# Kernel optimization log

Measured on AMD Instinct MI355X. Metric: run time of the kernel, lower is better.

## Reference

```python
import jax, jax.numpy as jnp
import numpy as np

B, T, C, H, N = 4, 4096, 1024, 16, 64
D_DECAY, D_AAA, D_MV, D_GATE = 64, 64, 32, 160
EPS_GN = 1e-5 * 8 ** 2  # GroupNorm eps = 1e-5 * head_size_divisor**2


def _k(i):
    return jax.random.fold_in(jax.random.key(0), i)


def setup_inputs():
    p = {}
    p["x"] = jax.random.normal(_k(1), (B, T, C), jnp.float32)
    p["v_first"] = jax.random.normal(_k(2), (B, T, C), jnp.float32)
    for i, name in enumerate(["x_r", "x_w", "x_k", "x_v", "x_a", "x_g"]):
        p[name] = jax.random.uniform(_k(10 + i), (1, 1, C), jnp.float32)
    p["w0"] = jnp.linspace(-7.0, -2.0, C, dtype=jnp.float32).reshape(1, 1, C) + 0.5
    p["w1"] = jax.random.normal(_k(20), (C, D_DECAY), jnp.float32) * 0.02
    p["w2"] = jax.random.normal(_k(21), (D_DECAY, C), jnp.float32) * 0.02
    p["a0"] = jax.random.normal(_k(22), (1, 1, C), jnp.float32) * 0.02
    p["a1"] = jax.random.normal(_k(23), (C, D_AAA), jnp.float32) * 0.02
    p["a2"] = jax.random.normal(_k(24), (D_AAA, C), jnp.float32) * 0.02
    p["v0"] = jnp.ones((1, 1, C), jnp.float32)
    p["v1"] = jax.random.normal(_k(25), (C, D_MV), jnp.float32) * 0.02
    p["v2"] = jax.random.normal(_k(26), (D_MV, C), jnp.float32) * 0.02
    p["g1"] = jax.random.normal(_k(27), (C, D_GATE), jnp.float32) * 0.02
    p["g2"] = jax.random.normal(_k(28), (D_GATE, C), jnp.float32) * 0.02
    p["k_k"] = jnp.full((1, 1, C), 0.85, jnp.float32)
    p["k_a"] = jnp.ones((1, 1, C), jnp.float32)
    p["r_k"] = jax.random.normal(_k(29), (H, N), jnp.float32) * 0.02
    s = 0.5 / C ** 0.5
    p["Wr"] = jax.random.uniform(_k(30), (C, C), jnp.float32, -s, s)
    p["Wk"] = jax.random.uniform(_k(31), (C, C), jnp.float32, -0.1 * s, 0.1 * s)
    p["Wv"] = jax.random.uniform(_k(32), (C, C), jnp.float32, -s, s)
    p["Wo"] = jax.random.uniform(_k(33), (C, C), jnp.float32, -s, s)
    p["ln_w"] = jnp.ones((C,), jnp.float32)
    p["ln_b"] = jnp.zeros((C,), jnp.float32)
    p["alpha"] = jnp.array(0.5, jnp.float32)
    return p


def _wkv_scan(ins, reverse):
    # ins: tuple of time-major (T,B,H,N) arrays: r, decay, k, v, a, b
    def step(S, inp):
        r_t, d_t, k_t, v_t, a_t, b_t = inp
        sa = jnp.einsum('bhij,bhj->bhi', S, a_t)  # in-context removal term
        S = (S * d_t[:, :, None, :]
             + sa[..., None] * b_t[:, :, None, :]
             + v_t[..., None] * k_t[:, :, None, :])
        return S, jnp.einsum('bhij,bhj->bhi', S, r_t)
    S0 = jnp.zeros((B, H, N, N), jnp.float32)
    return jax.lax.scan(step, S0, ins, reverse=reverse)[1]


def reference(x, v_first, x_r, x_w, x_k, x_v, x_a, x_g, w0, w1, w2, a0, a1, a2,
              v0, v1, v2, g1, g2, k_k, k_a, r_k, Wr, Wk, Wv, Wo, ln_w, ln_b, alpha):
    xx = jnp.pad(x, ((0, 0), (1, 0), (0, 0)))[:, :T, :] - x  # token shift
    xr = x + xx * x_r
    xw = x + xx * x_w
    xk = x + xx * x_k
    xv = x + xx * x_v
    xa = x + xx * x_a
    xg = x + xx * x_g
    r = xr @ Wr.T
    w = -jax.nn.softplus(-(w0 + jnp.tanh(xw @ w1) @ w2)) - 0.5
    k = xk @ Wk.T
    v = xv @ Wv.T
    v = v + (v_first - v) * jax.nn.sigmoid(v0 + (xv @ v1) @ v2)  # layer_id != 0
    a = jax.nn.sigmoid(a0 + (xa @ a1) @ a2)
    g = jax.nn.sigmoid(xg @ g1) @ g2
    kk = (k * k_k).reshape(B, T, H, N)
    kk = kk / jnp.maximum(jnp.linalg.norm(kk, axis=-1, keepdims=True), 1e-12)
    k = k * (1.0 + (a - 1.0) * k_a)
    rh = r.reshape(B, T, H, N)
    kh = k.reshape(B, T, H, N)
    vh = v.reshape(B, T, H, N)
    dec = jnp.exp(-jnp.exp(w.reshape(B, T, H, N)))  # per-channel decay
    ah = -kk
    bh = kk * a.reshape(B, T, H, N)
    tm = lambda z: jnp.transpose(z, (1, 0, 2, 3))  # -> (T,B,H,N)
    ins = (tm(rh), tm(dec), tm(kh), tm(vh), tm(ah), tm(bh))
    y_f = _wkv_scan(ins, reverse=False)
    y_b = _wkv_scan(ins, reverse=True)
    y = alpha * y_f + (1.0 - alpha) * y_b  # bidirectional blend (alpha)
    y = jnp.transpose(y, (1, 0, 2, 3))  # (B,T,H,N)
    mu = y.mean(-1, keepdims=True)
    var = y.var(-1, keepdims=True)
    y = (y - mu) / jnp.sqrt(var + EPS_GN)  # GroupNorm(H groups)
    y = y * ln_w.reshape(1, 1, H, N) + ln_b.reshape(1, 1, H, N)
    y = y + (rh * kh * r_k).sum(-1, keepdims=True) * vh
    out = (y.reshape(B, T, C) * g) @ Wo.T
    return (out, v_first)
```

## Files before the change

kernel.cpp:

```cpp
#include <hip/hip_runtime.h>
#include <hip/hip_bf16.h>
#include <math.h>

#define BB 4
#define TT 4096
#define CC 1024
#define HH 16
#define NN 64
#define BT (BB*TT)
#define EPS_GN 6.4e-4f
#define TMAX (TT-1)
#define LCH 64
#define STR 68
#define STR2 36

typedef __attribute__((ext_vector_type(8))) short bf16x8;
typedef __attribute__((ext_vector_type(4))) float f32x4;

__device__ __forceinline__ float sigmoidf_(float x) {
    return 1.0f / (1.0f + expf(-x));
}

__device__ __forceinline__ float waveReduceSum(float v) {
    #pragma unroll
    for (int off = 32; off > 0; off >>= 1)
        v += __shfl_xor(v, off, 64);
    return v;
}

__device__ __forceinline__ unsigned short f2bf(float f) {
    unsigned u = __float_as_uint(f);
    u += 0x7FFFu + ((u >> 16) & 1u);
    return (unsigned short)(u >> 16);
}
__device__ __forceinline__ float bf2f(unsigned short h) {
    return __uint_as_float(((unsigned)h) << 16);
}

__device__ __forceinline__ void gll16(const unsigned short* g, unsigned short* l) {
    __builtin_amdgcn_global_load_lds(
        (__attribute__((address_space(1))) void*)(g),
        (__attribute__((address_space(3))) void*)(l), 16, 0, 0);
}

template<int SA0,int SA1,int SB0,int SB1>
__device__ __forceinline__ void gemm64(const float* __restrict__ A,
                                       const float* __restrict__ B,
                                       float acc[4][4], int tr, int tc) {
    #pragma unroll 2
    for (int kx = 0; kx < 64; kx += 4) {
        float a_[4][4];
        if (SA0 == 1) {
            #pragma unroll
            for (int kk = 0; kk < 4; kk++) {
                float4 t = *(const float4*)&A[tr + (kx + kk) * SA1];
                a_[0][kk] = t.x; a_[1][kk] = t.y; a_[2][kk] = t.z; a_[3][kk] = t.w;
            }
        } else {
            #pragma unroll
            for (int r = 0; r < 4; r++) {
                float4 t = *(const float4*)&A[(tr + r) * SA0 + kx];
                a_[r][0] = t.x; a_[r][1] = t.y; a_[r][2] = t.z; a_[r][3] = t.w;
            }
        }
        float b_[4][4];
        if (SB0 == 1) {
            #pragma unroll
            for (int kk = 0; kk < 4; kk++) {
                float4 t = *(const float4*)&B[tc + (kx + kk) * SB1];
                b_[0][kk] = t.x; b_[1][kk] = t.y; b_[2][kk] = t.z; b_[3][kk] = t.w;
            }
        } else {
            #pragma unroll
            for (int cq = 0; cq < 4; cq++) {
                float4 t = *(const float4*)&B[(tc + cq) * SB0 + kx];
                b_[cq][0] = t.x; b_[cq][1] = t.y; b_[cq][2] = t.z; b_[cq][3] = t.w;
            }
        }
        #pragma unroll
        for (int r = 0; r < 4; r++)
            #pragma unroll
            for (int cq = 0; cq < 4; cq++)
                #pragma unroll
                for (int kk = 0; kk < 4; kk++)
                    acc[r][cq] = fmaf(a_[r][kk], b_[cq][kk], acc[r][cq]);
    }
}

__global__ __launch_bounds__(256) void conv_split_x6(
    const float* __restrict__ X,
    const float* __restrict__ mr, const float* __restrict__ mk,
    const float* __restrict__ mv, const float* __restrict__ mw,
    const float* __restrict__ ma, const float* __restrict__ mg,
    unsigned short* __restrict__ rH, unsigned short* __restrict__ rL,
    unsigned short* __restrict__ kH, unsigned short* __restrict__ kL,
    unsigned short* __restrict__ vH, unsigned short* __restrict__ vL,
    unsigned short* __restrict__ wH, unsigned short* __restrict__ wL,
    unsigned short* __restrict__ aH, unsigned short* __restrict__ aL,
    unsigned short* __restrict__ gH, unsigned short* __restrict__ gL)
{
    int g = blockIdx.x * 256 + threadIdx.x;
    int m = g >> 7;
    int k = (g & 127) * 8;
    const float* px = X + (size_t)m * CC + k;
    float xv8[8], pv[8];
    {
        float4 x0 = *(const float4*)px;
        float4 x1 = *(const float4*)(px + 4);
        xv8[0]=x0.x; xv8[1]=x0.y; xv8[2]=x0.z; xv8[3]=x0.w;
        xv8[4]=x1.x; xv8[5]=x1.y; xv8[6]=x1.z; xv8[7]=x1.w;
    }
    if ((m & (TT - 1)) == 0) {
        #pragma unroll
        for (int j = 0; j < 8; j++) pv[j] = 0.f;
    } else {
        float4 p0 = *(const float4*)(px - CC);
        float4 p1 = *(const float4*)(px - CC + 4);
        pv[0]=p0.x; pv[1]=p0.y; pv[2]=p0.z; pv[3]=p0.w;
        pv[4]=p1.x; pv[5]=p1.y; pv[6]=p1.z; pv[7]=p1.w;
    }
    const float* mixes[6] = {mr, mk, mv, mw, ma, mg};
    unsigned short* His[6] = {rH, kH, vH, wH, aH, gH};
    unsigned short* Los[6] = {rL, kL, vL, wL, aL, gL};
    for (int s = 0; s < 6; s++) {
        float4 m0 = *(const float4*)(mixes[s] + k);
        float4 m1 = *(const float4*)(mixes[s] + k + 4);
        float mv8[8] = {m0.x,m0.y,m0.z,m0.w,m1.x,m1.y,m1.z,m1.w};
        unsigned short hi[8], lo[8];
        #pragma unroll
        for (int j = 0; j < 8; j++) {
            float a = xv8[j] + (pv[j] - xv8[j]) * mv8[j];
            hi[j] = f2bf(a);
            lo[j] = f2bf(a - bf2f(hi[j]));
        }
        uint4 H, L;
        H.x = (unsigned)hi[0] | ((unsigned)hi[1] << 16);
        H.y = (unsigned)hi[2] | ((unsigned)hi[3] << 16);
        H.z = (unsigned)hi[4] | ((unsigned)hi[5] << 16);
        H.w = (unsigned)hi[6] | ((unsigned)hi[7] << 16);
        L.x = (unsigned)lo[0] | ((unsigned)lo[1] << 16);
        L.y = (unsigned)lo[2] | ((unsigned)lo[3] << 16);
        L.z = (unsigned)lo[4] | ((unsigned)lo[5] << 16);
        L.w = (unsigned)lo[6] | ((unsigned)lo[7] << 16);
        *(uint4*)(His[s] + (size_t)g * 8) = H;
        *(uint4*)(Los[s] + (size_t)g * 8) = L;
    }
}

__global__ __launch_bounds__(256) void conv_w4(
    const float* __restrict__ Wr, const float* __restrict__ Wk,
    const float* __restrict__ Wv, const float* __restrict__ Wo,
    unsigned short* __restrict__ Hi, unsigned short* __restrict__ Lo)
{
    int g = blockIdx.x * 256 + threadIdx.x;
    int y = blockIdx.y;
    const float* W = (y == 0) ? Wr : (y == 1) ? Wk : (y == 2) ? Wv : Wo;
    size_t doff = (size_t)y * CC * CC;
    int m = g >> 7;
    int k = (g & 127) * 8;
    const float* px = W + (size_t)m * CC + k;
    float a[8];
    {
        float4 x0 = *(const float4*)px;
        float4 x1 = *(const float4*)(px + 4);
        a[0]=x0.x; a[1]=x0.y; a[2]=x0.z; a[3]=x0.w;
        a[4]=x1.x; a[5]=x1.y; a[6]=x1.z; a[7]=x1.w;
    }
    unsigned short hi[8], lo[8];
    #pragma unroll
    for (int j = 0; j < 8; j++) {
        hi[j] = f2bf(a[j]);
        lo[j] = f2bf(a[j] - bf2f(hi[j]));
    }
    uint4 H, L;
    H.x = (unsigned)hi[0] | ((unsigned)hi[1] << 16);
    H.y = (unsigned)hi[2] | ((unsigned)hi[3] << 16);
    H.z = (unsigned)hi[4] | ((unsigned)hi[5] << 16);
    H.w = (unsigned)hi[6] | ((unsigned)hi[7] << 16);
    L.x = (unsigned)lo[0] | ((unsigned)lo[1] << 16);
    L.y = (unsigned)lo[2] | ((unsigned)lo[3] << 16);
    L.z = (unsigned)lo[4] | ((unsigned)lo[5] << 16);
    L.w = (unsigned)lo[6] | ((unsigned)lo[7] << 16);
    *(uint4*)(Hi + doff + (size_t)g * 8) = H;
    *(uint4*)(Lo + doff + (size_t)g * 8) = L;
}

__global__ __launch_bounds__(256) void conv_w1y(
    const float* __restrict__ w1, const float* __restrict__ a1,
    const float* __restrict__ v1, const float* __restrict__ g1,
    unsigned short* __restrict__ w1th, unsigned short* __restrict__ w1tl,
    unsigned short* __restrict__ a1th, unsigned short* __restrict__ a1tl,
    unsigned short* __restrict__ v1th, unsigned short* __restrict__ v1tl,
    unsigned short* __restrict__ g1th, unsigned short* __restrict__ g1tl)
{
    const int y = blockIdx.y;
    const float* W = (y == 0) ? w1 : (y == 1) ? a1 : (y == 2) ? v1 : g1;
    unsigned short* Hi = (y == 0) ? w1th : (y == 1) ? a1th : (y == 2) ? v1th : g1th;
    unsigned short* Lo = (y == 0) ? w1tl : (y == 1) ? a1tl : (y == 2) ? v1tl : g1tl;
    const int N    = (y == 2) ? 32 : (y == 3) ? 160 : 64;
    const int Npad = (y == 3) ? 192 : 64;
    int idx = blockIdx.x * 256 + threadIdx.x;
    if (idx >= Npad * 128) return;
    int n = idx >> 7, k0 = (idx & 127) * 8;
    unsigned short h8[8], l8[8];
    #pragma unroll
    for (int j = 0; j < 8; j++) {
        int k = k0 + j;
        float v = (n < N) ? W[(size_t)k * N + n] : 0.f;
        h8[j] = f2bf(v);
        l8[j] = f2bf(v - bf2f(h8[j]));
    }
    uint4 H, L;
    H.x = (unsigned)h8[0] | ((unsigned)h8[1] << 16);
    H.y = (unsigned)h8[2] | ((unsigned)h8[3] << 16);
    H.z = (unsigned)h8[4] | ((unsigned)h8[5] << 16);
    H.w = (unsigned)h8[6] | ((unsigned)h8[7] << 16);
    L.x = (unsigned)l8[0] | ((unsigned)l8[1] << 16);
    L.y = (unsigned)l8[2] | ((unsigned)l8[3] << 16);
    L.z = (unsigned)l8[4] | ((unsigned)l8[5] << 16);
    L.w = (unsigned)l8[6] | ((unsigned)l8[7] << 16);
    *(uint4*)(Hi + (size_t)n * CC + k0) = H;
    *(uint4*)(Lo + (size_t)n * CC + k0) = L;
}

__global__ __launch_bounds__(256) void conv_w2y(
    const float* __restrict__ w2, const float* __restrict__ a2,
    const float* __restrict__ v2, const float* __restrict__ g2,
    unsigned short* __restrict__ w2th, unsigned short* __restrict__ w2tl,
    unsigned short* __restrict__ a2th, unsigned short* __restrict__ a2tl,
    unsigned short* __restrict__ v2th, unsigned short* __restrict__ v2tl,
    unsigned short* __restrict__ g2th, unsigned short* __restrict__ g2tl)
{
    const int y = blockIdx.y;
    const float* W = (y == 0) ? w2 : (y == 1) ? a2 : (y == 2) ? v2 : g2;
    unsigned short* Hi = (y == 0) ? w2th : (y == 1) ? a2th : (y == 2) ? v2th : g2th;
    unsigned short* Lo = (y == 0) ? w2tl : (y == 1) ? a2tl : (y == 2) ? v2tl : g2tl;
    const int K  = (y == 2) ? 32 : (y == 3) ? 160 : 64;
    const int Kp = (y == 3) ? 192 : 64;
    int idx = blockIdx.x * 256 + threadIdx.x;
    int nk8 = Kp >> 3;
    if (idx >= CC * nk8) return;
    int n = idx / nk8, k0 = (idx - n * nk8) * 8;
    unsigned short h8[8], l8[8];
    #pragma unroll
    for (int j = 0; j < 8; j++) {
        int k = k0 + j;
        float v = (k < K) ? W[(size_t)k * CC + n] : 0.f;
        h8[j] = f2bf(v);
        l8[j] = f2bf(v - bf2f(h8[j]));
    }
    uint4 H, L;
    H.x = (unsigned)h8[0] | ((unsigned)h8[1] << 16);
    H.y = (unsigned)h8[2] | ((unsigned)h8[3] << 16);
    H.z = (unsigned)h8[4] | ((unsigned)h8[5] << 16);
    H.w = (unsigned)h8[6] | ((unsigned)h8[7] << 16);
    L.x = (unsigned)l8[0] | ((unsigned)l8[1] << 16);
    L.y = (unsigned)l8[2] | ((unsigned)l8[3] << 16);
    L.z = (unsigned)l8[4] | ((unsigned)l8[5] << 16);
    L.w = (unsigned)l8[6] | ((unsigned)l8[7] << 16);
    *(uint4*)(Hi + (size_t)n * Kp + k0) = H;
    *(uint4*)(Lo + (size_t)n * Kp + k0) = L;
}

__global__ __launch_bounds__(256, 3) void gemm_split_bf16(
    const unsigned short* __restrict__ A0h, const unsigned short* __restrict__ A0l,
    const unsigned short* __restrict__ A1h, const unsigned short* __restrict__ A1l,
    const unsigned short* __restrict__ A2h, const unsigned short* __restrict__ A2l,
    const unsigned short* __restrict__ W4h, const unsigned short* __restrict__ W4l,
    float* __restrict__ O0, float* __restrict__ O1, float* __restrict__ O2,
    int wbase)
{
    __shared__ __align__(16) unsigned short lds[4][128 * 32];
    const int sel = blockIdx.y;
    const unsigned short* Ah = (sel == 0) ? A0h : (sel == 1) ? A1h : A2h;
    const unsigned short* Al = (sel == 0) ? A0l : (sel == 1) ? A1l : A2l;
    float* Out = (sel == 0) ? O0 : (sel == 1) ? O1 : O2;
    const unsigned short* Bh = W4h + (size_t)(wbase + sel) * CC * CC;
    const unsigned short* Bl = W4l + (size_t)(wbase + sel) * CC * CC;
    const int tid = threadIdx.x, lane = tid & 63, wave = tid >> 6;
    const int wm = (wave >> 1) * 64, wn = (wave & 1) * 64;
    const int wg = blockIdx.x;
    const int xcd = wg & 7;
    const int j = wg >> 3;
    const int m0 = ((j >> 3) * 8 + xcd) * 128;
    const int n0 = (j & 7) * 128;

    f32x4 acc[4][4];
    #pragma unroll
    for (int i = 0; i < 4; i++)
        #pragma unroll
        for (int jj = 0; jj < 4; jj++)
            acc[i][jj] = (f32x4){0.f, 0.f, 0.f, 0.f};

    for (int k0 = 0; k0 < CC; k0 += 32) {
        #pragma unroll
        for (int p = 0; p < 4; p++) {
            const unsigned short* sbase = (p == 0) ? Ah : (p == 1) ? Al
                                        : (p == 2) ? Bh : Bl;
            const int rbase = (p < 2) ? m0 : n0;
            #pragma unroll
            for (int i = 0; i < 2; i++) {
                int slot = i * 256 + wave * 64 + lane;
                int row = slot >> 2, gsl = slot & 3;
                const unsigned short* src = sbase
                    + (size_t)(rbase + row) * CC + k0 + ((gsl ^ (row & 3)) * 8);
                gll16(src, &lds[p][(size_t)(i * 256 + wave * 64) * 8]);
            }
        }
        __syncthreads();

        const int gk = lane >> 4;
        bf16x8 bhf[4], blf[4];
        #pragma unroll
        for (int nt = 0; nt < 4; nt++) {
            int col = wn + nt * 16 + (lane & 15);
            int el = col * 32 + ((gk ^ (col & 3)) * 8);
            bhf[nt] = *(const bf16x8*)&lds[2][el];
// ... 109 lines not shown
            #pragma unroll
            for (int nt = 0; nt < 2; nt++) {
                acc[mt][nt] = __builtin_amdgcn_mfma_f32_16x16x32_bf16(
                    ahf, bhf[nt], acc[mt][nt], 0, 0, 0);
                acc[mt][nt] = __builtin_amdgcn_mfma_f32_16x16x32_bf16(
                    alf, bhf[nt], acc[mt][nt], 0, 0, 0);
                acc[mt][nt] = __builtin_amdgcn_mfma_f32_16x16x32_bf16(
                    ahf, blf[nt], acc[mt][nt], 0, 0, 0);
            }
        }
        __syncthreads();
    }
    #pragma unroll
    for (int mt = 0; mt < 4; mt++)
        #pragma unroll
        for (int nt = 0; nt < 2; nt++) {
            int col = n0 + wn + nt * 16 + (lane & 15);
            #pragma unroll
            for (int r = 0; r < 4; r++) {
                int row = m0 + wm + mt * 16 + (lane >> 4) * 4 + r;
                float v = acc[mt][nt][r];
                if (epi == 1) v = tanhf(v);
                else if (epi == 2) v = sigmoidf_(v);
                unsigned short h = f2bf(v);
                size_t off = (size_t)row * Kp + col;
                Oh[off] = h;
                Ol[off] = f2bf(v - bf2f(h));
            }
        }
}

__global__ __launch_bounds__(256, 3) void lora2_mfma(
    const unsigned short* __restrict__ awh, const unsigned short* __restrict__ awl,
    const unsigned short* __restrict__ aah, const unsigned short* __restrict__ aal,
    const unsigned short* __restrict__ avh, const unsigned short* __restrict__ avl,
    const unsigned short* __restrict__ agh, const unsigned short* __restrict__ agl,
    const unsigned short* __restrict__ w2h, const unsigned short* __restrict__ w2l,
    const unsigned short* __restrict__ a2h, const unsigned short* __restrict__ a2l,
    const unsigned short* __restrict__ v2h, const unsigned short* __restrict__ v2l,
    const unsigned short* __restrict__ g2h, const unsigned short* __restrict__ g2l,
    const float* __restrict__ w0, const float* __restrict__ a0v,
    const float* __restrict__ v0v, const float* __restrict__ v_first,
    float* __restrict__ decb, float* __restrict__ ab,
    float* __restrict__ vbuf, float* __restrict__ gb)
{
    __shared__ __align__(16) unsigned short lds[24576];
    const int z = blockIdx.z;
    const unsigned short *Ah, *Al, *Bh, *Bl; int Kp;
    if (z == 0)      { Ah = awh; Al = awl; Bh = w2h; Bl = w2l; Kp = 64;  }
    else if (z == 1) { Ah = aah; Al = aal; Bh = a2h; Bl = a2l; Kp = 64;  }
    else if (z == 2) { Ah = avh; Al = avl; Bh = v2h; Bl = v2l; Kp = 64;  }
    else             { Ah = agh; Al = agl; Bh = g2h; Bl = g2l; Kp = 192; }

    const int tid = threadIdx.x, lane = tid & 63, wave = tid >> 6;
    const int wm = (wave >> 1) * 64, wn = (wave & 1) * 32;
    const int m0 = blockIdx.x * 128, n0 = blockIdx.y * 64;

    f32x4 acc[4][2];
    #pragma unroll
    for (int i = 0; i < 4; i++)
        #pragma unroll
        for (int jj = 0; jj < 2; jj++)
            acc[i][jj] = (f32x4){0.f, 0.f, 0.f, 0.f};

    for (int k0 = 0; k0 < Kp; k0 += 64) {
        #pragma unroll
        for (int p = 0; p < 2; p++) {
            const unsigned short* sbase = (p == 0) ? Ah : Al;
            #pragma unroll
            for (int i = 0; i < 4; i++) {
                int slot = i * 256 + wave * 64 + lane;
                int row = slot >> 3, gsl = slot & 7;
                const unsigned short* src = sbase
                    + (size_t)(m0 + row) * Kp + k0 + ((gsl ^ (row & 7)) * 8);
                gll16(src, &lds[(size_t)(p * 8192) + (size_t)(i * 256 + wave * 64) * 8]);
            }
        }
        #pragma unroll
        for (int p = 0; p < 2; p++) {
            const unsigned short* sbase = (p == 0) ? Bh : Bl;
            #pragma unroll
            for (int i = 0; i < 2; i++) {
                int slot = i * 256 + wave * 64 + lane;
                int row = slot >> 3, gsl = slot & 7;
                const unsigned short* src = sbase
                    + (size_t)(n0 + row) * Kp + k0 + ((gsl ^ (row & 7)) * 8);
                gll16(src, &lds[(size_t)(16384 + p * 4096) + (size_t)(i * 256 + wave * 64) * 8]);
            }
        }
        __syncthreads();

        #pragma unroll
        for (int ks = 0; ks < 2; ks++) {
            bf16x8 bhf[2], blf[2];
            #pragma unroll
            for (int nt = 0; nt < 2; nt++) {
                int col = wn + nt * 16 + (lane & 15);
                int gk = ks * 4 + (lane >> 4);
                int el = col * 64 + ((gk ^ (col & 7)) * 8);
                bhf[nt] = *(const bf16x8*)&lds[16384 + el];
                blf[nt] = *(const bf16x8*)&lds[20480 + el];
            }
            #pragma unroll
            for (int mt = 0; mt < 4; mt++) {
                int row = wm + mt * 16 + (lane & 15);
                int gk = ks * 4 + (lane >> 4);
                int el = row * 64 + ((gk ^ (row & 7)) * 8);
                bf16x8 ahf = *(const bf16x8*)&lds[el];
                bf16x8 alf = *(const bf16x8*)&lds[8192 + el];
                #pragma unroll
                for (int nt = 0; nt < 2; nt++) {
                    acc[mt][nt] = __builtin_amdgcn_mfma_f32_16x16x32_bf16(
                        ahf, bhf[nt], acc[mt][nt], 0, 0, 0);
                    acc[mt][nt] = __builtin_amdgcn_mfma_f32_16x16x32_bf16(
                        alf, bhf[nt], acc[mt][nt], 0, 0, 0);
                    acc[mt][nt] = __builtin_amdgcn_mfma_f32_16x16x32_bf16(
                        ahf, blf[nt], acc[mt][nt], 0, 0, 0);
                }
            }
        }
        __syncthreads();
    }
    float* cf = (float*)&lds[0];
    #pragma unroll
    for (int mt = 0; mt < 4; mt++)
        #pragma unroll
        for (int nt = 0; nt < 2; nt++)
            #pragma unroll
            for (int r = 0; r < 4; r++) {
                int row = wm + mt * 16 + (lane >> 4) * 4 + r;
                int col = wn + nt * 16 + (lane & 15);
                cf[row * 68 + col] = acc[mt][nt][r];
            }
    __syncthreads();
    #pragma unroll
    for (int i = 0; i < 8; i++) {
        int idx = tid + 256 * i;
        int row = idx >> 4, c4 = (idx & 15) * 4;
        float4 v = *(float4*)&cf[row * 68 + c4];
        int gm = m0 + row;
        int c = n0 + c4;
        size_t off = (size_t)gm * CC + c;
        if (z == 0) {
            float4 w0q = *(const float4*)(w0 + c);
            float4 o;
            o.x = expf(-expf(-log1pf(expf(-(w0q.x + v.x))) - 0.5f));
            o.y = expf(-expf(-log1pf(expf(-(w0q.y + v.y))) - 0.5f));
            o.z = expf(-expf(-log1pf(expf(-(w0q.z + v.z))) - 0.5f));
            o.w = expf(-expf(-log1pf(expf(-(w0q.w + v.w))) - 0.5f));
            *(float4*)&decb[off] = o;
        } else if (z == 1) {
            float4 a0q = *(const float4*)(a0v + c);
            float4 o;
            o.x = sigmoidf_(a0q.x + v.x);
            o.y = sigmoidf_(a0q.y + v.y);
            o.z = sigmoidf_(a0q.z + v.z);
            o.w = sigmoidf_(a0q.w + v.w);
            *(float4*)&ab[off] = o;
        } else if (z == 2) {
            float4 v0q = *(const float4*)(v0v + c);
            float4 vr = *(const float4*)&vbuf[off];
            float4 vf = *(const float4*)&v_first[off];
            float4 o;
            o.x = vr.x + (vf.x - vr.x) * sigmoidf_(v0q.x + v.x);
            o.y = vr.y + (vf.y - vr.y) * sigmoidf_(v0q.y + v.y);
            o.z = vr.z + (vf.z - vr.z) * sigmoidf_(v0q.z + v.z);
            o.w = vr.w + (vf.w - vr.w) * sigmoidf_(v0q.w + v.w);
            *(float4*)&vbuf[off] = o;
        } else {
            *(float4*)&gb[off] = v;
        }
    }
}

template<int CBT>
__global__ __launch_bounds__(256, 3) void wkvA(
    const float* __restrict__ kb, const float* __restrict__ ab,
    const float* __restrict__ vb, const float* __restrict__ decb,
    const float* __restrict__ k_k, const float* __restrict__ k_a,
    float* __restrict__ Gb, float* __restrict__ Ub,
    float* __restrict__ Bpb, float* __restrict__ Kpb,
    float* __restrict__ wcb, int cb)
{
    __shared__ __align__(16) float sA[64 * STR];
    __shared__ __align__(16) float sO[64 * STR];
    __shared__ __align__(16) float sT[64 * STR];
    __shared__ float sSeg[4][64];
    const int inst = blockIdx.x;
    const int bhd = inst / CBT, lc = inst % CBT;
    const int dir = bhd & 1, bh = bhd >> 1, b = bh >> 4, h = bh & 15;
    const int c64 = (cb * CBT + lc) * LCH;
    const int tid = threadIdx.x;
    const int lane = tid & 63, seg = tid >> 6;
    const int ch = h * 64 + lane;
    const size_t gbase = (size_t)inst * 4096;

    float loc[16];
    {
        float run = 1.f;
        #pragma unroll
        for (int i = 0; i < 16; i++) {
            int p = seg * 16 + i;
            int t = dir ? (TMAX - (c64 + p)) : (c64 + p);
            float d = decb[((size_t)(b * TT + t)) * CC + ch];
            run *= d; loc[i] = run;
        }
        sSeg[seg][lane] = run;
    }
    __syncthreads();
    float pre = 1.f;
    for (int s2 = 0; s2 < seg; ++s2) pre *= sSeg[s2][lane];
    float kreg[16];
    {
        const float kkl = k_k[ch], kal = k_a[ch];
        #pragma unroll
        for (int i = 0; i < 16; i++) {
            int p = seg * 16 + i;
            int t = dir ? (TMAX - (c64 + p)) : (c64 + p);
            size_t ra = ((size_t)(b * TT + t)) * CC + ch;
            float kraw = kb[ra], asig = ab[ra];
            float kkv = kraw * kkl;
            float s2 = waveReduceSum(kkv * kkv);
            float kkn = kkv / fmaxf(sqrtf(s2), 1e-12f);
            float wc = loc[i] * pre;
            float wx = (i == 0) ? pre : loc[i - 1] * pre;
            float apv = -kkn * wx;
            float bpv = kkn * asig / wc;
            float kpv = kraw * (1.f + (asig - 1.f) * kal) / wc;
            sA[lane * STR + p] = apv;
            sO[lane * STR + p] = bpv;
            kreg[i] = kpv;
            Gb[gbase + p * 64 + lane] = apv;
            Bpb[gbase + p * 64 + lane] = bpv;
            Kpb[gbase + p * 64 + lane] = kpv;
            wcb[gbase + p * 64 + lane] = wc;
        }
    }
    __syncthreads();

    const int tr = (tid >> 4) * 4, tc = (tid & 15) * 4;
    {
        float acc[4][4] = {};
        gemm64<1, STR, 1, STR>(sA, sO, acc, tr, tc);
        #pragma unroll
        for (int r = 0; r < 4; r++)
            #pragma unroll
            for (int cq = 0; cq < 4; cq++)
                sT[(tr + r) * STR + tc + cq] = (tc + cq < tr + r) ? acc[r][cq] : 0.f;
    }
    __syncthreads();
    #pragma unroll
    for (int i = 0; i < 16; i++)
        sO[lane * STR + seg * 16 + i] = kreg[i];
    __syncthreads();
    {
        float acc[4][4] = {};
        gemm64<1, STR, 1, STR>(sA, sO, acc, tr, tc);
        __syncthreads();
        #pragma unroll
        for (int r = 0; r < 4; r++)
            #pragma unroll
            for (int cq = 0; cq < 4; cq++)
                sA[(tr + r) * STR + tc + cq] = (tc + cq < tr + r) ? acc[r][cq] : 0.f;
    }
    __syncthreads();
    {
        float accY[4][4] = {};
        const float* vbase = vb + ((size_t)(b * TT + (dir ? (TMAX - c64) : c64))) * CC
                           + h * 64 + tc;
        const ptrdiff_t vstep = dir ? -(ptrdiff_t)CC : (ptrdiff_t)CC;
        #pragma unroll 2
        for (int j4 = 0; j4 < 64; j4 += 4) {
            float a_[4][4];
            #pragma unroll
            for (int r = 0; r < 4; r++) {
                float4 t4 = *(const float4*)&sA[(tr + r) * STR + j4];
                a_[r][0] = t4.x; a_[r][1] = t4.y; a_[r][2] = t4.z; a_[r][3] = t4.w;
            }
            float4 vq[4];
            #pragma unroll
            for (int kk = 0; kk < 4; kk++)
                vq[kk] = *(const float4*)(vbase + (ptrdiff_t)(j4 + kk) * vstep);
            #pragma unroll
            for (int r = 0; r < 4; r++) {
                accY[r][0] = fmaf(a_[r][0], vq[0].x, fmaf(a_[r][1], vq[1].x,
                             fmaf(a_[r][2], vq[2].x, fmaf(a_[r][3], vq[3].x, accY[r][0]))));
                accY[r][1] = fmaf(a_[r][0], vq[0].y, fmaf(a_[r][1], vq[1].y,
                             fmaf(a_[r][2], vq[2].y, fmaf(a_[r][3], vq[3].y, accY[r][1]))));
                accY[r][2] = fmaf(a_[r][0], vq[0].z, fmaf(a_[r][1], vq[1].z,
                             fmaf(a_[r][2], vq[2].z, fmaf(a_[r][3], vq[3].z, accY[r][2]))));
                accY[r][3] = fmaf(a_[r][0], vq[0].w, fmaf(a_[r][1], vq[1].w,
                             fmaf(a_[r][2], vq[2].w, fmaf(a_[r][3], vq[3].w, accY[r][3]))));
            }
        }
        __syncthreads();
        #pragma unroll
        for (int r = 0; r < 4; r++)
            #pragma unroll
            for (int cq = 0; cq < 4; cq++)
                sO[(tr + r) * STR + tc + cq] = accY[r][cq];
    }
    __syncthreads();
    if (tid < 64) {
        for (int r = 0; r < 64; ++r) {
            float acc = 0.f;
            for (int s = 0; s < r; ++s)
                acc = fmaf(sT[r * STR + s], sA[s * STR + tid], acc);
            sA[r * STR + tid] = (r == tid) ? 1.f : acc;
        }
    }
    __syncthreads();
    {
        float accU[4][4] = {};
        gemm64<STR, 1, 1, STR>(sA, sO, accU, tr, tc);
        float accG[4][4] = {};
        gemm64<STR, 1, 1, 64>(sA, Gb + gbase, accG, tr, tc);
        __syncthreads();
        #pragma unroll
        for (int r = 0; r < 4; r++) {
            *(float4*)&Gb[gbase + (tr + r) * 64 + tc] =
                make_float4(accG[r][0], accG[r][1], accG[r][2], accG[r][3]);
            *(float4*)&Ub[gbase + (tr + r) * 64 + tc] =
                make_float4(accU[r][0], accU[r][1], accU[r][2], accU[r][3]);
        }
    }
}

template<int CBT>
__global__ __launch_bounds__(256) void wkvB(
    const float* __restrict__ vb,
    const float* __restrict__ Gb, float* __restrict__ Ub,
    const float* __restrict__ Bpb, const float* __restrict__ Kpb,
    const float* __restrict__ wcb, float* __restrict__ S0b,
    float* __restrict__ Scur, int cb)
{
    __shared__ __align__(16) float sG[64 * STR];
    __shared__ __align__(16) float sB[64 * STR];
    __shared__ __align__(16) float sK[64 * STR];
    __shared__ __align__(16) float sS[32 * STR];
    __shared__ __align__(16) float sU[64 * STR2];
    __shared__ __align__(16) float sV[64 * STR2];
    const int blk = blockIdx.x;
    const int bhd = blk >> 1, half = blk & 1;
    const int dir = bhd & 1, bh = bhd >> 1, b = bh >> 4, h = bh & 15;
    const int tid = threadIdx.x;
    const int i0 = half * 32;

    for (int i = tid; i < 2048; i += 256) {
        int rr = i >> 6, jj = i & 63;
        sS[rr * STR + jj] = Scur[(size_t)bhd * 4096 + (size_t)(i0 + rr) * 64 + jj];
    }
    __syncthreads();

    for (int lc = 0; lc < CBT; ++lc) {
        const int inst = bhd * CBT + lc;
        const size_t gbase = (size_t)inst * 4096;
        const int c64 = (cb * CBT + lc) * LCH;
        for (int i = tid; i < 4096; i += 256) {
            int rr = i >> 6, jj = i & 63;
            sG[rr * STR + jj] = Gb[gbase + i];
            sB[rr * STR + jj] = Bpb[gbase + i];
            sK[rr * STR + jj] = Kpb[gbase + i];
        }
        for (int i = tid; i < 2048; i += 256) {
            int s = i >> 5, ii = i & 31;
            int t = dir ? (TMAX - (c64 + s)) : (c64 + s);
            sV[s * STR2 + ii] = vb[((size_t)(b * TT + t)) * CC + h * 64 + i0 + ii];
        }
        for (int i = tid; i < 2048; i += 256) {
            int rr = i >> 6, jj = i & 63;
            S0b[gbase + (size_t)(i0 + rr) * 64 + jj] = sS[rr * STR + jj];
        }
        __syncthreads();
        {
            const int ts = (tid >> 4) * 4;
            const int ti = (tid & 15) * 2;
            float acc[4][2];
            #pragma unroll
            for (int r = 0; r < 4; r++) {
                acc[r][0] = Ub[gbase + (size_t)(ts + r) * 64 + i0 + ti];
                acc[r][1] = Ub[gbase + (size_t)(ts + r) * 64 + i0 + ti + 1];
            }
            #pragma unroll 2
            for (int j4 = 0; j4 < 64; j4 += 4) {
                float4 g0 = *(const float4*)&sG[(ts + 0) * STR + j4];
                float4 g1 = *(const float4*)&sG[(ts + 1) * STR + j4];
                float4 g2 = *(const float4*)&sG[(ts + 2) * STR + j4];
                float4 g3 = *(const float4*)&sG[(ts + 3) * STR + j4];
                float4 s0 = *(const float4*)&sS[(ti) * STR + j4];
                float4 s1 = *(const float4*)&sS[(ti + 1) * STR + j4];
                acc[0][0] = fmaf(g0.x,s0.x,fmaf(g0.y,s0.y,fmaf(g0.z,s0.z,fmaf(g0.w,s0.w,acc[0][0]))));
                acc[0][1] = fmaf(g0.x,s1.x,fmaf(g0.y,s1.y,fmaf(g0.z,s1.z,fmaf(g0.w,s1.w,acc[0][1]))));
                acc[1][0] = fmaf(g1.x,s0.x,fmaf(g1.y,s0.y,fmaf(g1.z,s0.z,fmaf(g1.w,s0.w,acc[1][0]))));
                acc[1][1] = fmaf(g1.x,s1.x,fmaf(g1.y,s1.y,fmaf(g1.z,s1.z,fmaf(g1.w,s1.w,acc[1][1]))));
                acc[2][0] = fmaf(g2.x,s0.x,fmaf(g2.y,s0.y,fmaf(g2.z,s0.z,fmaf(g2.w,s0.w,acc[2][0]))));
                acc[2][1] = fmaf(g2.x,s1.x,fmaf(g2.y,s1.y,fmaf(g2.z,s1.z,fmaf(g2.w,s1.w,acc[2][1]))));
                acc[3][0] = fmaf(g3.x,s0.x,fmaf(g3.y,s0.y,fmaf(g3.z,s0.z,fmaf(g3.w,s0.w,acc[3][0]))));
                acc[3][1] = fmaf(g3.x,s1.x,fmaf(g3.y,s1.y,fmaf(g3.z,s1.z,fmaf(g3.w,s1.w,acc[3][1]))));
            }
            #pragma unroll
            for (int r = 0; r < 4; r++) {
                sU[(ts + r) * STR2 + ti]     = acc[r][0];
                sU[(ts + r) * STR2 + ti + 1] = acc[r][1];
                Ub[gbase + (size_t)(ts + r) * 64 + i0 + ti]     = acc[r][0];
                Ub[gbase + (size_t)(ts + r) * 64 + i0 + ti + 1] = acc[r][1];
            }
        }
        __syncthreads();
        {
            const int ti = (tid >> 4) * 2;
            const int tj = (tid & 15) * 4;
            float acc[2][4] = {};
            for (int s = 0; s < 64; ++s) {
                float u0 = sU[s * STR2 + ti], u1 = sU[s * STR2 + ti + 1];
                float v0 = sV[s * STR2 + ti], v1 = sV[s * STR2 + ti + 1];
                float4 bq = *(const float4*)&sB[s * STR + tj];
                float4 kq = *(const float4*)&sK[s * STR + tj];
                acc[0][0] = fmaf(u0, bq.x, fmaf(v0, kq.x, acc[0][0]));
                acc[0][1] = fmaf(u0, bq.y, fmaf(v0, kq.y, acc[0][1]));
                acc[0][2] = fmaf(u0, bq.z, fmaf(v0, kq.z, acc[0][2]));
                acc[0][3] = fmaf(u0, bq.w, fmaf(v0, kq.w, acc[0][3]));
                acc[1][0] = fmaf(u1, bq.x, fmaf(v1, kq.x, acc[1][0]));
                acc[1][1] = fmaf(u1, bq.y, fmaf(v1, kq.y, acc[1][1]));
                acc[1][2] = fmaf(u1, bq.z, fmaf(v1, kq.z, acc[1][2]));
                acc[1][3] = fmaf(u1, bq.w, fmaf(v1, kq.w, acc[1][3]));
            }
            float w63[4];
            #pragma unroll
            for (int cq = 0; cq < 4; cq++)
                w63[cq] = wcb[gbase + 63 * 64 + tj + cq];
            #pragma unroll
            for (int r = 0; r < 2; r++)
                #pragma unroll
                for (int cq = 0; cq < 4; cq++) {
                    float sv = sS[(ti + r) * STR + tj + cq];
                    sS[(ti + r) * STR + tj + cq] = (sv + acc[r][cq]) * w63[cq];
                }
        }
        __syncthreads();
    }
    for (int i = tid; i < 2048; i += 256)
        Scur[(size_t)bhd * 4096 + (size_t)(i0 + (i >> 6)) * 64 + (i & 63)]
            = sS[(i >> 6) * STR + (i & 63)];
}

template<int CBT>
__global__ __launch_bounds__(256) void wkvC(
    const float* __restrict__ rb, const float* __restrict__ vb,
    const float* __restrict__ Bpb, const float* __restrict__ Kpb,
    const float* __restrict__ Ub, const float* __restrict__ S0b,
    const float* __restrict__ wcb, const float* __restrict__ alpha_p,
    float* __restrict__ yb, int cb)
{
    __shared__ __align__(16) float sR[64 * STR];
    __shared__ __align__(16) float sO[64 * STR];
    __shared__ __align__(16) float sT2[64 * STR];
    const int inst = blockIdx.x;
    const int bhd = inst / CBT, lc = inst % CBT;
    const int dir = bhd & 1, bh = bhd >> 1, b = bh >> 4, h = bh & 15;
    const int c64 = (cb * CBT + lc) * LCH;
    const int tid = threadIdx.x, lane = tid & 63, seg = tid >> 6;
    const size_t gbase = (size_t)inst * 4096;
    const float alpha = alpha_p[0];
    const float wscale = dir ? (1.f - alpha) : alpha;
    const bool first = (cb < (32 / CBT));

    #pragma unroll
    for (int i = 0; i < 16; i++) {
        int p = seg * 16 + i;
        int t = dir ? (TMAX - (c64 + p)) : (c64 + p);
        size_t ra = ((size_t)(b * TT + t)) * CC + h * 64 + lane;
        float wc = wcb[gbase + p * 64 + lane];
        sR[lane * STR + p] = rb[ra] * wc;
        sO[lane * STR + p] = Bpb[gbase + p * 64 + lane];
    }
    __syncthreads();
    const int tr = (tid >> 4) * 4, tc = (tid & 15) * 4;
    float accO[4][4] = {};
    {
        float acc[4][4] = {};
        gemm64<1, STR, 1, STR>(sR, sO, acc, tr, tc);
        #pragma unroll
        for (int r = 0; r < 4; r++)
            #pragma unroll
            for (int cq = 0; cq < 4; cq++)
                sT2[(tr + r) * STR + tc + cq] = (tc + cq <= tr + r) ? acc[r][cq] : 0.f;
    }
    __syncthreads();
    for (int i = tid; i < 4096; i += 256)
        sO[(i >> 6) * STR + (i & 63)] = Ub[gbase + i];
    __syncthreads();
    gemm64<STR, 1, 1, STR>(sT2, sO, accO, tr, tc);
    __syncthreads();
    #pragma unroll
    for (int i = 0; i < 16; i++) {
        int p = seg * 16 + i;
        sO[lane * STR + p] = Kpb[gbase + p * 64 + lane];
    }
    __syncthreads();
    {
        float acc[4][4] = {};
        gemm64<1, STR, 1, STR>(sR, sO, acc, tr, tc);
        #pragma unroll
        for (int r = 0; r < 4; r++)
            #pragma unroll
            for (int cq = 0; cq < 4; cq++)
                sT2[(tr + r) * STR + tc + cq] = (tc + cq <= tr + r) ? acc[r][cq] : 0.f;
    }
    __syncthreads();
    #pragma unroll
    for (int i = 0; i < 16; i++) {
        int p = seg * 16 + i;
        int t = dir ? (TMAX - (c64 + p)) : (c64 + p);
        sO[p * STR + lane] = vb[((size_t)(b * TT + t)) * CC + h * 64 + lane];
    }
    __syncthreads();
    gemm64<STR, 1, 1, STR>(sT2, sO, accO, tr, tc);
    __syncthreads();
    for (int i = tid; i < 4096; i += 256)
        sO[(i >> 6) * STR + (i & 63)] = S0b[gbase + i];
    __syncthreads();
    gemm64<1, STR, STR, 1>(sR, sO, accO, tr, tc);
    #pragma unroll
    for (int r = 0; r < 4; r++) {
        int p = tr + r;
        int t = dir ? (TMAX - (c64 + p)) : (c64 + p);
        float* yp = &yb[((size_t)(b * TT + t)) * CC + h * 64 + tc];
        float4 o;
        if (first) {
            o.x = wscale * accO[r][0];
            o.y = wscale * accO[r][1];
            o.z = wscale * accO[r][2];
            o.w = wscale * accO[r][3];
        } else {
            float4 old = *(float4*)yp;
            o.x = old.x + wscale * accO[r][0];
            o.y = old.y + wscale * accO[r][1];
            o.z = old.z + wscale * accO[r][2];
            o.w = old.w + wscale * accO[r][3];
        }
        *(float4*)yp = o;
    }
}

__global__ __launch_bounds__(256) void post_kernel(
    const float* __restrict__ yb, const float* __restrict__ rbv,
    const float* __restrict__ kbv, const float* __restrict__ abv,
    const float* __restrict__ vbv, const float* __restrict__ gbv,
    const float* __restrict__ kaw, const float* __restrict__ r_k,
    const float* __restrict__ ln_w, const float* __restrict__ ln_b,
    unsigned short* __restrict__ zh, unsigned short* __restrict__ zl)
{
    const int t = blockIdx.x;
    const int tid = threadIdx.x;
    const size_t base = (size_t)t * CC;
    #pragma unroll
    for (int j = 0; j < 4; j++) {
        int c = tid + 256 * j;
        float y = yb[base + c];
        float s1 = waveReduceSum(y);
        float s2 = waveReduceSum(y * y);
        float mu = s1 * (1.0f / 64.0f);
        float var = s2 * (1.0f / 64.0f) - mu * mu;
        float yn = (y - mu) * rsqrtf(var + EPS_GN);
        yn = yn * ln_w[c] + ln_b[c];
        float rv = rbv[base + c];
        float kf = kbv[base + c] * (1.0f + (abv[base + c] - 1.0f) * kaw[c]);
        float vv = vbv[base + c];
        float dot = waveReduceSum(rv * kf * r_k[c]);
        yn += dot * vv;
        float z = yn * gbv[base + c];
        unsigned short h = f2bf(z);
        zh[base + c] = h;
        zl[base + c] = f2bf(z - bf2f(h));
    }
}

extern "C" void kernel_launch(void* const* d_in, const int* in_sizes, int n_in,
                              void* d_out, int out_size, void* d_ws, size_t ws_size,
                              hipStream_t stream)
{
    (void)in_sizes; (void)n_in; (void)out_size;
    const float* x      = (const float*)d_in[0];
    const float* vfirst = (const float*)d_in[1];
    const float* x_r    = (const float*)d_in[2];
    const float* x_w    = (const float*)d_in[3];
    const float* x_k    = (const float*)d_in[4];
    const float* x_v    = (const float*)d_in[5];
    const float* x_a    = (const float*)d_in[6];
    const float* x_g    = (const float*)d_in[7];
    const float* w0     = (const float*)d_in[8];
    const float* w1     = (const float*)d_in[9];
    const float* w2     = (const float*)d_in[10];
    const float* a0     = (const float*)d_in[11];
    const float* a1     = (const float*)d_in[12];
    const float* a2     = (const float*)d_in[13];
    const float* v0     = (const float*)d_in[14];
    const float* v1     = (const float*)d_in[15];
    const float* v2     = (const float*)d_in[16];
    const float* g1     = (const float*)d_in[17];
    const float* g2     = (const float*)d_in[18];
    const float* k_k    = (const float*)d_in[19];
    const float* k_a    = (const float*)d_in[20];
    const float* r_k    = (const float*)d_in[21];
    const float* Wr     = (const float*)d_in[22];
    const float* Wk     = (const float*)d_in[23];
    const float* Wv     = (const float*)d_in[24];
    const float* Wo     = (const float*)d_in[25];
    const float* ln_w   = (const float*)d_in[26];
    const float* ln_b   = (const float*)d_in[27];
    const float* alpha  = (const float*)d_in[28];

    const bool big = (ws_size >= 600ull * 1000 * 1000);
    const int  cbt = big ? 16 : 8;
    const int  nb  = 64 / cbt;
    const size_t CHB = (size_t)128 * cbt * 4096;

    const size_t SZ = (size_t)BT * CC;
    float* ws   = (float*)d_ws;
    float* rb   = ws + 0 * SZ;
    float* kb   = ws + 1 * SZ;
    float* vb   = ws + 2 * SZ;
    float* decb = ws + 3 * SZ;
    float* ab   = ws + 4 * SZ;
    float* actf = ws + 5 * SZ;
    unsigned short* awh = (unsigned short*)actf;
    unsigned short* awl = awh + (size_t)BT * 64;
    unsigned short* aah = awl + (size_t)BT * 64;
    unsigned short* aal = aah + (size_t)BT * 64;
    unsigned short* avh = aal + (size_t)BT * 64;
    unsigned short* avl = avh + (size_t)BT * 64;
    unsigned short* agh = avl + (size_t)BT * 64;
    unsigned short* agl = agh + (size_t)BT * 192;
    float* Gb   = actf + (size_t)BT * 384;
    float* Ub   = Gb + CHB;
    float* Bpb  = Ub + CHB;
    float* Kpb  = Bpb + CHB;
    float* S0b  = Kpb + CHB;
    float* wcb  = S0b + CHB;
    float* Scur = wcb + CHB;
    unsigned short* W4h = (unsigned short*)(Scur + (size_t)128 * 4096);
    unsigned short* W4l = W4h + (size_t)CC * CC * 4;
    unsigned short* w2th = W4l + (size_t)CC * CC * 4;
    unsigned short* w2tl = w2th + (size_t)CC * 64;
    unsigned short* a2th = w2tl + (size_t)CC * 64;
    unsigned short* a2tl = a2th + (size_t)CC * 64;
    unsigned short* v2th = a2tl + (size_t)CC * 64;
    unsigned short* v2tl = v2th + (size_t)CC * 64;
    unsigned short* g2th = v2tl + (size_t)CC * 64;
    unsigned short* g2tl = g2th + (size_t)CC * 192;
    unsigned short* w1th = g2tl + (size_t)CC * 192;
    unsigned short* w1tl = w1th + (size_t)64 * CC;
    unsigned short* a1th = w1tl + (size_t)64 * CC;
    unsigned short* a1tl = a1th + (size_t)64 * CC;
    unsigned short* v1th = a1tl + (size_t)64 * CC;
    unsigned short* v1tl = v1th + (size_t)64 * CC;
    unsigned short* g1th = v1tl + (size_t)64 * CC;
    unsigned short* g1tl = g1th + (size_t)192 * CC;
    float* outp = (float*)d_out;
    unsigned short* xrh = (unsigned short*)outp;
    unsigned short* xrl = xrh + SZ;
    unsigned short* xkh = xrl + SZ;
    unsigned short* xkl = xkh + SZ;
    unsigned short* xvh = (unsigned short*)decb;
    unsigned short* xvl = xvh + SZ;
    unsigned short* xwh = (unsigned short*)rb;
    unsigned short* xwl = xwh + SZ;
    unsigned short* xah = (unsigned short*)kb;
    unsigned short* xal = xah + SZ;
    unsigned short* xgh = (unsigned short*)vb;
    unsigned short* xgl = xgh + SZ;
    float* gb   = outp;
    float* yb   = outp + SZ;
    unsigned short* zAh = (unsigned short*)decb;
    unsigned short* zAl = zAh + SZ;

    dim3 blk(256);
    const int NG_A = BT * (CC / 8);
    dim3 gridA(NG_A / 256);

    conv_split_x6<<<gridA, blk, 0, stream>>>(x, x_r, x_k, x_v, x_w, x_a, x_g,
        xrh, xrl, xkh, xkl, xvh, xvl, xwh, xwl, xah, xal, xgh, xgl);
    conv_w4<<<dim3(512, 4), blk, 0, stream>>>(Wr, Wk, Wv, Wo, W4h, W4l);
    conv_w1y<<<dim3(96, 4), blk, 0, stream>>>(w1, a1, v1, g1,
        w1th, w1tl, a1th, a1tl, v1th, v1tl, g1th, g1tl);
    conv_w2y<<<dim3(96, 4), blk, 0, stream>>>(w2, a2, v2, g2,
        w2th, w2tl, a2th, a2tl, v2th, v2tl, g2th, g2tl);

    lora1_mfma<<<dim3(BT / 128, 6), blk, 0, stream>>>(
        xwh, xwl, xah, xal, xvh, xvl, xgh, xgl,
        w1th, w1tl, a1th, a1tl, v1th, v1tl, g1th, g1tl,
        awh, awl, aah, aal, avh, avl, agh, agl);

    gemm_split_bf16<<<dim3(1024, 3), blk, 0, stream>>>(
        xrh, xrl, xkh, xkl, xvh, xvl, W4h, W4l, rb, kb, vb, 0);

    lora2_mfma<<<dim3(BT / 128, CC / 64, 4), blk, 0, stream>>>(
        awh, awl, aah, aal, avh, avl, agh, agl,
        w2th, w2tl, a2th, a2tl, v2th, v2tl, g2th, g2tl,
        w0, a0, v0, vfirst, decb, ab, vb, gb);

    hipMemsetAsync(Scur, 0, (size_t)128 * 4096 * sizeof(float), stream);
    if (big) {
        for (int cb = 0; cb < 4; ++cb) {
            wkvA<16><<<dim3(2048), blk, 0, stream>>>(kb, ab, vb, decb, k_k, k_a,
                                                     Gb, Ub, Bpb, Kpb, wcb, cb);
            wkvB<16><<<dim3(256), blk, 0, stream>>>(vb, Gb, Ub, Bpb, Kpb, wcb,
                                                    S0b, Scur, cb);
            wkvC<16><<<dim3(2048), blk, 0, stream>>>(rb, vb, Bpb, Kpb, Ub, S0b,
                                                     wcb, alpha, yb, cb);
        }
    } else {
        for (int cb = 0; cb < 8; ++cb) {
            wkvA<8><<<dim3(1024), blk, 0, stream>>>(kb, ab, vb, decb, k_k, k_a,
                                                    Gb, Ub, Bpb, Kpb, wcb, cb);
            wkvB<8><<<dim3(256), blk, 0, stream>>>(vb, Gb, Ub, Bpb, Kpb, wcb,
                                                   S0b, Scur, cb);
            wkvC<8><<<dim3(1024), blk, 0, stream>>>(rb, vb, Bpb, Kpb, Ub, S0b,
                                                    wcb, alpha, yb, cb);
        }
    }
    (void)nb;

    post_kernel<<<dim3(BT), blk, 0, stream>>>(yb, rb, kb, ab, vb, gb, k_a, r_k,
                                              ln_w, ln_b, zAh, zAl);
    hipMemcpyAsync(outp + SZ, vfirst, SZ * sizeof(float),
                   hipMemcpyDeviceToDevice, stream);
    gemm_split_bf16<<<dim3(1024, 1), blk, 0, stream>>>(
        zAh, zAl, zAh, zAl, zAh, zAl, W4h, W4l, outp, outp, outp, 3);
}
```

Baseline: 2.956 ms.

## Split wkvB state rows across four blocks and register-cache triangular solve

The sequential chunk-state kernel wkvB now splits each head's 64-row state into four 16-row slices instead of two 32-row halves, so twice as many blocks (512) run the serial chunk recurrence with less work per thread. Shared buffers shrink to match. Separately, the triangular forward-substitution in wkvA now keeps the solved column in a fully unrolled register array with two accumulators instead of re-reading shared memory. The trade-offs are that each wkvB block reloads the full G/B/K chunk matrices for a smaller slice, which adds redundant traffic, and the 64-float register array may raise register pressure in wkvA.

Result: faster. 2.662 ms (-9.9%).

```diff
diff --git a/kernel.cpp b/kernel.cpp
--- a/kernel.cpp
+++ b/kernel.cpp
@@ -12,7 +12,7 @@
 #define TMAX (TT-1)
 #define LCH 64
 #define STR 68
-#define STR2 36
+#define STR3 20
 
 typedef __attribute__((ext_vector_type(8))) short bf16x8;
 typedef __attribute__((ext_vector_type(4))) float f32x4;
@@ -728,12 +728,22 @@
     }
     __syncthreads();
     if (tid < 64) {
+        float y[64];
+        #pragma unroll
         for (int r = 0; r < 64; ++r) {
-            float acc = 0.f;
-            for (int s = 0; s < r; ++s)
-                acc = fmaf(sT[r * STR + s], sA[s * STR + tid], acc);
-            sA[r * STR + tid] = (r == tid) ? 1.f : acc;
-        }
+            float a0 = 0.f, a1 = 0.f;
+            #pragma unroll
+            for (int s = 0; s + 1 < r; s += 2) {
+                a0 = fmaf(sT[r * STR + s],     y[s],     a0);
+                a1 = fmaf(sT[r * STR + s + 1], y[s + 1], a1);
+            }
+            if (r & 1)
+                a0 = fmaf(sT[r * STR + (r - 1)], y[r - 1], a0);
+            y[r] = (r == tid) ? 1.f : (a0 + a1);
+        }
+        #pragma unroll
+        for (int r = 0; r < 64; ++r)
+            sA[r * STR + tid] = y[r];
     }
     __syncthreads();
     {
@@ -763,16 +773,16 @@
     __shared__ __align__(16) float sG[64 * STR];
     __shared__ __align__(16) float sB[64 * STR];
     __shared__ __align__(16) float sK[64 * STR];
-    __shared__ __align__(16) float sS[32 * STR];
-    __shared__ __align__(16) float sU[64 * STR2];
-    __shared__ __align__(16) float sV[64 * STR2];
+    __shared__ __align__(16) float sS[16 * STR];
+    __shared__ __align__(16) float sU[64 * STR3];
+    __shared__ __align__(16) float sV[64 * STR3];
     const int blk = blockIdx.x;
-    const int bhd = blk >> 1, half = blk & 1;
+    const int bhd = blk >> 2, q = blk & 3;
     const int dir = bhd & 1, bh = bhd >> 1, b = bh >> 4, h = bh & 15;
     const int tid = threadIdx.x;
-    const int i0 = half * 32;
-
-    for (int i = tid; i < 2048; i += 256) {
+    const int i0 = q * 16;
+
+    for (int i = tid; i < 1024; i += 256) {
         int rr = i >> 6, jj = i & 63;
         sS[rr * STR + jj] = Scur[(size_t)bhd * 4096 + (size_t)(i0 + rr) * 64 + jj];
     }
@@ -788,84 +798,69 @@
             sB[rr * STR + jj] = Bpb[gbase + i];
             sK[rr * STR + jj] = Kpb[gbase + i];
         }
-        for (int i = tid; i < 2048; i += 256) {
-            int s = i >> 5, ii = i & 31;
+        for (int i = tid; i < 1024; i += 256) {
+            int s = i >> 4, ii = i & 15;
             int t = dir ? (TMAX - (c64 + s)) : (c64 + s);
-            sV[s * STR2 + ii] = vb[((size_t)(b * TT + t)) * CC + h * 64 + i0 + ii];
-        }
-        for (int i = tid; i < 2048; i += 256) {
+            sV[s * STR3 + ii] = vb[((size_t)(b * TT + t)) * CC + h * 64 + i0 + ii];
+        }
+        for (int i = tid; i < 1024; i += 256) {
             int rr = i >> 6, jj = i & 63;
             S0b[gbase + (size_t)(i0 + rr) * 64 + jj] = sS[rr * STR + jj];
         }
         __syncthreads();
         {
             const int ts = (tid >> 4) * 4;
-            const int ti = (tid & 15) * 2;
-            float acc[4][2];
-            #pragma unroll
-            for (int r = 0; r < 4; r++) {
-                acc[r][0] = Ub[gbase + (size_t)(ts + r) * 64 + i0 + ti];
-                acc[r][1] = Ub[gbase + (size_t)(ts + r) * 64 + i0 + ti + 1];
-            }
+            const int ti = tid & 15;
+            float acc[4];
+            #pragma unroll
+            for (int r = 0; r < 4; r++)
+                acc[r] = Ub[gbase + (size_t)(ts + r) * 64 + i0 + ti];
             #pragma unroll 2
             for (int j4 = 0; j4 < 64; j4 += 4) {
                 float4 g0 = *(const float4*)&sG[(ts + 0) * STR + j4];
                 float4 g1 = *(const float4*)&sG[(ts + 1) * STR + j4];
                 float4 g2 = *(const float4*)&sG[(ts + 2) * STR + j4];
                 float4 g3 = *(const float4*)&sG[(ts + 3) * STR + j4];
-                float4 s0 = *(const float4*)&sS[(ti) * STR + j4];
-                float4 s1 = *(const float4*)&sS[(ti + 1) * STR + j4];
-                acc[0][0] = fmaf(g0.x,s0.x,fmaf(g0.y,s0.y,fmaf(g0.z,s0.z,fmaf(g0.w,s0.w,acc[0][0]))));
-                acc[0][1] = fmaf(g0.x,s1.x,fmaf(g0.y,s1.y,fmaf(g0.z,s1.z,fmaf(g0.w,s1.w,acc[0][1]))));
-                acc[1][0] = fmaf(g1.x,s0.x,fmaf(g1.y,s0.y,fmaf(g1.z,s0.z,fmaf(g1.w,s0.w,acc[1][0]))));
-                acc[1][1] = fmaf(g1.x,s1.x,fmaf(g1.y,s1.y,fmaf(g1.z,s1.z,fmaf(g1.w,s1.w,acc[1][1]))));
-                acc[2][0] = fmaf(g2.x,s0.x,fmaf(g2.y,s0.y,fmaf(g2.z,s0.z,fmaf(g2.w,s0.w,acc[2][0]))));
-                acc[2][1] = fmaf(g2.x,s1.x,fmaf(g2.y,s1.y,fmaf(g2.z,s1.z,fmaf(g2.w,s1.w,acc[2][1]))));
-                acc[3][0] = fmaf(g3.x,s0.x,fmaf(g3.y,s0.y,fmaf(g3.z,s0.z,fmaf(g3.w,s0.w,acc[3][0]))));
-                acc[3][1] = fmaf(g3.x,s1.x,fmaf(g3.y,s1.y,fmaf(g3.z,s1.z,fmaf(g3.w,s1.w,acc[3][1]))));
+                float4 sv = *(const float4*)&sS[ti * STR + j4];
+                acc[0] = fmaf(g0.x,sv.x,fmaf(g0.y,sv.y,fmaf(g0.z,sv.z,fmaf(g0.w,sv.w,acc[0]))));
+                acc[1] = fmaf(g1.x,sv.x,fmaf(g1.y,sv.y,fmaf(g1.z,sv.z,fmaf(g1.w,sv.w,acc[1]))));
+                acc[2] = fmaf(g2.x,sv.x,fmaf(g2.y,sv.y,fmaf(g2.z,sv.z,fmaf(g2.w,sv.w,acc[2]))));
+                acc[3] = fmaf(g3.x,sv.x,fmaf(g3.y,sv.y,fmaf(g3.z,sv.z,fmaf(g3.w,sv.w,acc[3]))));
             }
             #pragma unroll
             for (int r = 0; r < 4; r++) {
-                sU[(ts + r) * STR2 + ti]     = acc[r][0];
-                sU[(ts + r) * STR2 + ti + 1] = acc[r][1];
-                Ub[gbase + (size_t)(ts + r) * 64 + i0 + ti]     = acc[r][0];
-                Ub[gbase + (size_t)(ts + r) * 64 + i0 + ti + 1] = acc[r][1];
+                sU[(ts + r) * STR3 + ti] = acc[r];
+                Ub[gbase + (size_t)(ts + r) * 64 + i0 + ti] = acc[r];
             }
         }
         __syncthreads();
         {
-            const int ti = (tid >> 4) * 2;
+            const int ti = tid >> 4;
             const int tj = (tid & 15) * 4;
-            float acc[2][4] = {};
+            float acc[4] = {};
             for (int s = 0; s < 64; ++s) {
-                float u0 = sU[s * STR2 + ti], u1 = sU[s * STR2 + ti + 1];
-                float v0 = sV[s * STR2 + ti], v1 = sV[s * STR2 + ti + 1];
+                float u0 = sU[s * STR3 + ti];
+                float v0 = sV[s * STR3 + ti];
                 float4 bq = *(const float4*)&sB[s * STR + tj];
                 float4 kq = *(const float4*)&sK[s * STR + tj];
-                acc[0][0] = fmaf(u0, bq.x, fmaf(v0, kq.x, acc[0][0]));
-                acc[0][1] = fmaf(u0, bq.y, fmaf(v0, kq.y, acc[0][1]));
-                acc[0][2] = fmaf(u0, bq.z, fmaf(v0, kq.z, acc[0][2]));
-                acc[0][3] = fmaf(u0, bq.w, fmaf(v0, kq.w, acc[0][3]));
-                acc[1][0] = fmaf(u1, bq.x, fmaf(v1, kq.x, acc[1][0]));
-                acc[1][1] = fmaf(u1, bq.y, fmaf(v1, kq.y, acc[1][1]));
-                acc[1][2] = fmaf(u1, bq.z, fmaf(v1, kq.z, acc[1][2]));
-                acc[1][3] = fmaf(u1, bq.w, fmaf(v1, kq.w, acc[1][3]));
+                acc[0] = fmaf(u0, bq.x, fmaf(v0, kq.x, acc[0]));
+                acc[1] = fmaf(u0, bq.y, fmaf(v0, kq.y, acc[1]));
+                acc[2] = fmaf(u0, bq.z, fmaf(v0, kq.z, acc[2]));
+                acc[3] = fmaf(u0, bq.w, fmaf(v0, kq.w, acc[3]));
             }
             float w63[4];
             #pragma unroll
             for (int cq = 0; cq < 4; cq++)
                 w63[cq] = wcb[gbase + 63 * 64 + tj + cq];
             #pragma unroll
-            for (int r = 0; r < 2; r++)
-                #pragma unroll
-                for (int cq = 0; cq < 4; cq++) {
-                    float sv = sS[(ti + r) * STR + tj + cq];
-                    sS[(ti + r) * STR + tj + cq] = (sv + acc[r][cq]) * w63[cq];
-                }
+            for (int cq = 0; cq < 4; cq++) {
+                float sv = sS[ti * STR + tj + cq];
+                sS[ti * STR + tj + cq] = (sv + acc[cq]) * w63[cq];
+            }
         }
         __syncthreads();
     }
-    for (int i = tid; i < 2048; i += 256)
+    for (int i = tid; i < 1024; i += 256)
         Scur[(size_t)bhd * 4096 + (size_t)(i0 + (i >> 6)) * 64 + (i & 63)]
             = sS[(i >> 6) * STR + (i & 63)];
 }
@@ -1039,7 +1034,6 @@
 
     const bool big = (ws_size >= 600ull * 1000 * 1000);
     const int  cbt = big ? 16 : 8;
-    const int  nb  = 64 / cbt;
     const size_t CHB = (size_t)128 * cbt * 4096;
 
     const size_t SZ = (size_t)BT * CC;
@@ -1131,7 +1125,7 @@
         for (int cb = 0; cb < 4; ++cb) {
             wkvA<16><<<dim3(2048), blk, 0, stream>>>(kb, ab, vb, decb, k_k, k_a,
                                                      Gb, Ub, Bpb, Kpb, wcb, cb);
-            wkvB<16><<<dim3(256), blk, 0, stream>>>(vb, Gb, Ub, Bpb, Kpb, wcb,
+            wkvB<16><<<dim3(512), blk, 0, stream>>>(vb, Gb, Ub, Bpb, Kpb, wcb,
                                                     S0b, Scur, cb);
             wkvC<16><<<dim3(2048), blk, 0, stream>>>(rb, vb, Bpb, Kpb, Ub, S0b,
                                                      wcb, alpha, yb, cb);
@@ -1140,13 +1134,12 @@
         for (int cb = 0; cb < 8; ++cb) {
             wkvA<8><<<dim3(1024), blk, 0, stream>>>(kb, ab, vb, decb, k_k, k_a,
                                                     Gb, Ub, Bpb, Kpb, wcb, cb);
-            wkvB<8><<<dim3(256), blk, 0, stream>>>(vb, Gb, Ub, Bpb, Kpb, wcb,
+            wkvB<8><<<dim3(512), blk, 0, stream>>>(vb, Gb, Ub, Bpb, Kpb, wcb,
                                                    S0b, Scur, cb);
             wkvC<8><<<dim3(1024), blk, 0, stream>>>(rb, vb, Bpb, Kpb, Ub, S0b,
                                                     wcb, alpha, yb, cb);
         }
     }
-    (void)nb;
 
     post_kernel<<<dim3(BT), blk, 0, stream>>>(yb, rb, kb, ab, vb, gb, k_a, r_k,
                                               ln_w, ln_b, zAh, zAl);
```
